# Kernel optimization log

Hardware: AMD Instinct MI355X
Metric: run time of the kernel (lower is better)

The kernel has to match this reference:

```python
import jax, jax.numpy as jnp
import numpy as np

N = 50000
E = 1600000
IN_C = 128
HID = 128
OUT_C = 64


def setup_inputs() -> dict:
    key = jax.random.key(0)
    ks = jax.random.split(key, 10)
    x = jax.random.normal(ks[0], (N, IN_C), dtype=jnp.float32)
    edge_index = jax.random.randint(ks[1], (2, E), 0, N, dtype=jnp.int64)
    s = lambda fan_in: 1.0 / np.sqrt(fan_in)
    W1 = jax.random.uniform(ks[2], (HID, IN_C), jnp.float32, -s(IN_C), s(IN_C))
    b1 = jnp.zeros((HID,), jnp.float32)
    Wc = jax.random.uniform(ks[3], (HID, HID + IN_C), jnp.float32, -s(HID + IN_C), s(HID + IN_C))
    bc = jax.random.uniform(ks[4], (HID,), jnp.float32, -s(HID + IN_C), s(HID + IN_C))
    W2 = jax.random.uniform(ks[5], (HID, HID), jnp.float32, -s(HID), s(HID))
    b2 = jnp.zeros((HID,), jnp.float32)
    Wo = jax.random.uniform(ks[6], (OUT_C, 2 * HID), jnp.float32, -s(2 * HID), s(2 * HID))
    bo = jax.random.uniform(ks[7], (OUT_C,), jnp.float32, -s(2 * HID), s(2 * HID))
    return {"x": x, "edge_index": edge_index, "W1": W1, "b1": b1,
            "Wc": Wc, "bc": bc, "W2": W2, "b2": b2, "Wo": Wo, "bo": bo}


def _gcn_conv(x, src, dst, norm, W, b):
    # PyG GCNConv: h = x @ W^T, propagate with sym-norm coeffs, add bias.
    h = x @ W.T                                   # [N, F_out]
    msg = h[src] * norm[:, None]                  # gather + scale, [E+N, F_out]
    out = jax.ops.segment_sum(msg, dst, num_segments=N)  # scatter-add
    return out + b


def _norm_coeffs(edge_index):
    # add self-loops, then sym normalization: D^{-1/2} A_hat D^{-1/2}
    loop = jnp.arange(N, dtype=edge_index.dtype)
    src = jnp.concatenate([edge_index[0], loop])
    dst = jnp.concatenate([edge_index[1], loop])
    deg = jax.ops.segment_sum(jnp.ones_like(dst, dtype=jnp.float32), dst, num_segments=N)
    dis = jnp.where(deg > 0, jax.lax.rsqrt(deg), 0.0)
    norm = dis[src] * dis[dst]
    return src, dst, norm


def reference(x, edge_index, W1, b1, Wc, bc, W2, b2, Wo, bo):
    src, dst, norm = _norm_coeffs(edge_index)
    x_agg = jax.nn.relu(_gcn_conv(x, src, dst, norm, W1, b1))
    x_comb = jnp.concatenate([x_agg, x], axis=1)
    x_comb = jax.nn.relu(x_comb @ Wc.T + bc)
    # dropout is identity in eval mode
    x_agg2 = _gcn_conv(x_comb, src, dst, norm, W2, b2)
    x_out = jnp.concatenate([x_agg2, x_comb], axis=1)
    return x_out @ Wo.T + bo
```

## Files before the change

### kernel.cpp

```cpp
#include <hip/hip_runtime.h>
#include <hip/hip_fp16.h>

#define Nn 50000
#define Ee 1600000
#define NRANGE 196
#define CAP 10240
#define CHUNK 4096

typedef __attribute__((ext_vector_type(8))) short short8;
typedef __attribute__((ext_vector_type(4))) float f32x4;
typedef unsigned short ushort;
typedef unsigned int uint;

__device__ __forceinline__ ushort f32_to_bf16(float f) {
    unsigned u = __builtin_bit_cast(unsigned, f);
    unsigned r = u + 0x7FFFu + ((u >> 16) & 1u);
    return (ushort)(r >> 16);
}
__device__ __forceinline__ float bf16_to_f32(ushort h) {
    unsigned u = ((unsigned)h) << 16;
    return __builtin_bit_cast(float, u);
}


__global__ __launch_bounds__(256) void partition_kernel(const int* __restrict__ ei,
                                                        int* __restrict__ gcursor,
                                                        int2* __restrict__ buckets) {
    __shared__ int cnt[NRANGE];
    __shared__ int cur[NRANGE];
    int t = threadIdx.x;
    if (t < NRANGE) cnt[t] = 0;
    __syncthreads();
    int base = blockIdx.x * CHUNK;
    const int* __restrict__ dst = ei + Ee;
    #pragma unroll
    for (int k = 0; k < CHUNK / 256; ++k) {
        int e = base + k * 256 + t;
        if (e < Ee) atomicAdd(&cnt[dst[e] >> 8], 1);
    }
    __syncthreads();
    if (t < NRANGE) cur[t] = atomicAdd(&gcursor[t], cnt[t]);
    __syncthreads();
    #pragma unroll
    for (int k = 0; k < CHUNK / 256; ++k) {
        int e = base + k * 256 + t;
        if (e < Ee) {
            int d = dst[e];
            int r = d >> 8;
            int slot = atomicAdd(&cur[r], 1);
            if (slot < CAP) buckets[r * CAP + slot] = make_int2(ei[e], d);
        }
    }
}

__global__ __launch_bounds__(256) void count_kernel(const int2* __restrict__ buckets,
                                                    const int* __restrict__ gcursor,
                                                    int* __restrict__ counts,
                                                    float* __restrict__ dis) {
    __shared__ int cnt[256];
    int r = blockIdx.x, t = threadIdx.x;
    cnt[t] = 0;
    __syncthreads();
    int n = gcursor[r]; n = (n < CAP) ? n : CAP;
    const int2* b = buckets + (size_t)r * CAP;
    for (int i = t; i < n; i += 256) {
        int2 p = b[i];
        atomicAdd(&cnt[p.y & 255], 1);
    }
    __syncthreads();
    int node = r * 256 + t;
    if (node < Nn) {
        counts[node] = cnt[t];
        dis[node] = rsqrtf((float)(cnt[t] + 1));
    }
}

__global__ void scan1_kernel(const int* __restrict__ counts, int* __restrict__ offsets,
                             int* __restrict__ partials) {
    __shared__ int sd[256];
    int t = threadIdx.x;
    int i = blockIdx.x * 256 + t;
    int cp = 0;
    if (i < Nn) cp = (counts[i] + 7) & ~7;
    int v = cp;
    #pragma unroll
    for (int off = 1; off < 256; off <<= 1) {
        sd[t] = v; __syncthreads();
        int add = (t >= off) ? sd[t - off] : 0;
        __syncthreads();
        v += add;
    }
    if (i < Nn) offsets[i] = v - cp;
    if (t == 255) partials[blockIdx.x] = v;
}

__global__ void scan3_kernel(int* __restrict__ offsets, const int* __restrict__ partials,
                             const int* __restrict__ counts, int* __restrict__ csr) {
    __shared__ int sd[256];
    int t = threadIdx.x;
    int s = (t < blockIdx.x) ? partials[t] : 0;
    sd[t] = s; __syncthreads();
    #pragma unroll
    for (int off = 128; off > 0; off >>= 1) {
        if (t < off) sd[t] += sd[t + off];
        __syncthreads();
    }
    int base = sd[0];
    int i = blockIdx.x * 256 + t;
    if (i < Nn) {
        int off = offsets[i] + base;
        offsets[i] = off;
        int deg = counts[i];
        int cp  = (deg + 7) & ~7;
        for (int j = off + deg; j < off + cp; ++j) csr[j] = Nn;
        if (i == Nn - 1) offsets[Nn] = off + cp;
    }
}

__global__ __launch_bounds__(256) void fill_kernel(const int2* __restrict__ buckets,
                                                   const int* __restrict__ gcursor,
                                                   const int* __restrict__ offsets,
                                                   int* __restrict__ csr) {
    __shared__ int cur[256];
    int r = blockIdx.x, t = threadIdx.x;
    int node = r * 256 + t;
    cur[t] = (node < Nn) ? offsets[node] : 0;
    __syncthreads();
    int n = gcursor[r]; n = (n < CAP) ? n : CAP;
    const int2* b = buckets + (size_t)r * CAP;
    for (int i = t; i < n; i += 256) {
        int2 p = b[i];
        int pos = atomicAdd(&cur[p.y & 255], 1);
        csr[pos] = p.x;
    }
}

__global__ void prep_w_kernel(const float* __restrict__ W1, const float* __restrict__ Wc,
                              const float* __restrict__ W2, const float* __restrict__ Wo,
                              ushort* __restrict__ base) {
    int i = blockIdx.x * 256 + threadIdx.x;
    const float* src; ushort* hi; ushort* lo; int idx;
    if (i < 16384)      { src = W1; hi = base;          lo = base + 16384;  idx = i; }
    else if (i < 49152) { src = Wc; hi = base + 32768;  lo = base + 65536;  idx = i - 16384; }
    else if (i < 65536) { src = W2; hi = base + 98304;  lo = base + 114688; idx = i - 49152; }
    else                { src = Wo; hi = base + 131072; lo = base + 147456; idx = i - 65536; }
    float f = src[idx];
    ushort hb = f32_to_bf16(f);
    hi[idx] = hb;
    lo[idx] = f32_to_bf16(f - bf16_to_f32(hb));
}

__global__ void split_x_kernel(const float* __restrict__ x, ushort* __restrict__ xhi,
                               ushort* __restrict__ xlo) {
    int i = (blockIdx.x * 256 + threadIdx.x) * 4;
    float4 v = *(const float4*)(x + i);
    float vv[4] = {v.x, v.y, v.z, v.w};
    ushort h[4], l[4];
    #pragma unroll
    for (int j = 0; j < 4; ++j) {
        h[j] = f32_to_bf16(vv[j]);
        l[j] = f32_to_bf16(vv[j] - bf16_to_f32(h[j]));
    }
    *(uint2*)(xhi + i) = make_uint2((uint)h[0] | ((uint)h[1] << 16),
                                    (uint)h[2] | ((uint)h[3] << 16));
    *(uint2*)(xlo + i) = make_uint2((uint)l[0] | ((uint)l[1] << 16),
                                    (uint)l[2] | ((uint)l[3] << 16));
}

template <int CO, int K, bool RELU, bool HASBIAS, bool SCALEDIS, int OUTMODE>
__global__ __launch_bounds__(256, 3) void mfma_gemm(
    const ushort* __restrict__ AH0, const ushort* __restrict__ AL0,
    const ushort* __restrict__ AH1, const ushort* __restrict__ AL1,
    const ushort* __restrict__ Whi, const ushort* __restrict__ Wlo,
    const float* __restrict__ bias, const float* __restrict__ dis,
    void* __restrict__ outp, ushort* __restrict__ outLo) {
    constexpr int NF = CO / 16;
    constexpr int NCH = K / 64;
    constexpr int WISS = CO / 32;

    __shared__ ushort lds[2 * 64 * 64 + 2 * CO * 64];
    ushort* ldsAh = lds;
    ushort* ldsAl = lds + 64 * 64;
    ushort* ldsWh = lds + 2 * 64 * 64;
    ushort* ldsWl = ldsWh + CO * 64;

    int tid  = threadIdx.x;
    int wave = tid >> 6;
    int lane = tid & 63;
    int c = lane & 15;
    int g = lane >> 4;
    int row0 = blockIdx.x * 64;

    f32x4 acc1[NF], acc2[NF];
    #pragma unroll
    for (int f = 0; f < NF; ++f) {
        acc1[f] = (f32x4){0.f, 0.f, 0.f, 0.f};
        acc2[f] = (f32x4){0.f, 0.f, 0.f, 0.f};
    }

    #pragma unroll
    for (int ch = 0; ch < NCH; ++ch) {
        const int k0 = ch * 64;
        const ushort* Ah = (K == 256 && k0 >= 128) ? AH1 : AH0;
        const ushort* Al = (K == 256 && k0 >= 128) ? AL1 : AL0;
        const int kb = (K == 256 && k0 >= 128) ? (k0 - 128) : k0;

        #pragma unroll
        for (int i = 0; i < 2; ++i) {
            int idx = tid + i * 256;
            int row = idx >> 3, kg = idx & 7;
            int gr = row0 + row; gr = (gr < Nn) ? gr : (Nn - 1);
            int sb = (kg * 16) ^ ((row & 7) << 4);
            int ldsoff = (i * 256 + wave * 64) * 8;
            __builtin_amdgcn_global_load_lds(Ah + (size_t)gr * 128 + kb + (sb >> 1),
                                             &ldsAh[ldsoff], 16, 0, 0);
            __builtin_amdgcn_global_load_lds(Al + (size_t)gr * 128 + kb + (sb >> 1),
                                             &ldsAl[ldsoff], 16, 0, 0);
        }
        #pragma unroll
        for (int i = 0; i < WISS; ++i) {
            int idx = tid + i * 256;
            int col = idx >> 3, kg = idx & 7;
            int sb = (kg * 16) ^ ((col & 7) << 4);
            int ldsoff = (i * 256 + wave * 64) * 8;
            __builtin_amdgcn_global_load_lds(Whi + (size_t)col * K + k0 + (sb >> 1),
                                             &ldsWh[ldsoff], 16, 0, 0);
            __builtin_amdgcn_global_load_lds(Wlo + (size_t)col * K + k0 + (sb >> 1),
                                             &ldsWl[ldsoff], 16, 0, 0);
        }
        __syncthreads();

        #pragma unroll
        for (int s = 0; s < 2; ++s) {
            int arow = wave * 16 + c;
            int ab = (s * 64 + g * 16) ^ ((arow & 7) << 4);
            short8 ahi = *(const short8*)((const char*)ldsAh + arow * 128 + ab);
            short8 alo = *(const short8*)((const char*)ldsAl + arow * 128 + ab);
            #pragma unroll
            for (int f = 0; f < NF; ++f) {
                int col = f * 16 + c;
                int wb = (s * 64 + g * 16) ^ ((col & 7) << 4);
                short8 bh = *(const short8*)((const char*)ldsWh + col * 128 + wb);
                short8 bl = *(const short8*)((const char*)ldsWl + col * 128 + wb);
                acc1[f] = __builtin_amdgcn_mfma_f32_16x16x32_bf16(ahi, bh, acc1[f], 0, 0, 0);
                acc2[f] = __builtin_amdgcn_mfma_f32_16x16x32_bf16(ahi, bl, acc2[f], 0, 0, 0);
                acc2[f] = __builtin_amdgcn_mfma_f32_16x16x32_bf16(alo, bh, acc2[f], 0, 0, 0);
            }
        }
        __syncthreads();
    }

    #pragma unroll
    for (int f = 0; f < NF; ++f) {
        int col = f * 16 + c;
        float bv = HASBIAS ? bias[col] : 0.f;
        #pragma unroll
        for (int rg = 0; rg < 4; ++rg) {
            int row = row0 + wave * 16 + g * 4 + rg;
            if (row < Nn) {
                float v = acc1[f][rg] + acc2[f][rg] + bv;
                if (RELU) v = fmaxf(v, 0.f);
                if (SCALEDIS) v *= dis[row];
                size_t idx = (size_t)row * CO + col;
                if constexpr (OUTMODE == 1) {
                    ((__half*)outp)[idx] = __float2half_rn(v);
                } else if constexpr (OUTMODE == 2) {
                    ushort hb = f32_to_bf16(v);
                    ((ushort*)outp)[idx] = hb;
                    outLo[idx] = f32_to_bf16(v - bf16_to_f32(hb));
                } else {
                    ((float*)outp)[idx] = v;
                }
            }
        }
    }
}

template <bool RELU>
__global__ __launch_bounds__(256) void propagate_kernel(
    const __half* __restrict__ gbuf, const int* __restrict__ offs,
    const int* __restrict__ csr, const float* __restrict__ dis,
    const float* __restrict__ bias, ushort* __restrict__ outHi,
    ushort* __restrict__ outLo) {
    int node = blockIdx.x * 4 + (threadIdx.x >> 6);
    if (node >= Nn) return;
    int lane = threadIdx.x & 63;
    float2 sv = __half22float2(*((const __half2*)(gbuf + ((size_t)node << 7)) + lane));
    float ax = sv.x, ay = sv.y;
    int beg = offs[node], end = offs[node + 1];
    for (int e = beg; e < end; e += 8) {
        int s0 = csr[e],     s1 = csr[e + 1], s2 = csr[e + 2], s3 = csr[e + 3];
        int s4 = csr[e + 4], s5 = csr[e + 5], s6 = csr[e + 6], s7 = csr[e + 7];
        __half2 h0 = *((const __half2*)(gbuf + ((size_t)s0 << 7)) + lane);
        __half2 h1 = *((const __half2*)(gbuf + ((size_t)s1 << 7)) + lane);
        __half2 h2 = *((const __half2*)(gbuf + ((size_t)s2 << 7)) + lane);
        __half2 h3 = *((const __half2*)(gbuf + ((size_t)s3 << 7)) + lane);
        __half2 h4 = *((const __half2*)(gbuf + ((size_t)s4 << 7)) + lane);
        __half2 h5 = *((const __half2*)(gbuf + ((size_t)s5 << 7)) + lane);
        __half2 h6 = *((const __half2*)(gbuf + ((size_t)s6 << 7)) + lane);
        __half2 h7 = *((const __half2*)(gbuf + ((size_t)s7 << 7)) + lane);
        float2 v0 = __half22float2(h0), v1 = __half22float2(h1);
        float2 v2 = __half22float2(h2), v3 = __half22float2(h3);
        float2 v4 = __half22float2(h4), v5 = __half22float2(h5);
        float2 v6 = __half22float2(h6), v7 = __half22float2(h7);
        ax += ((v0.x + v1.x) + (v2.x + v3.x)) + ((v4.x + v5.x) + (v6.x + v7.x));
        ay += ((v0.y + v1.y) + (v2.y + v3.y)) + ((v4.y + v5.y) + (v6.y + v7.y));
    }
    float di = dis[node];
    ax = fmaf(di, ax, bias[lane * 2]);
    ay = fmaf(di, ay, bias[lane * 2 + 1]);
    if (RELU) { ax = fmaxf(ax, 0.f); ay = fmaxf(ay, 0.f); }
    ushort hx = f32_to_bf16(ax), hy = f32_to_bf16(ay);
    ushort lx = f32_to_bf16(ax - bf16_to_f32(hx));
    ushort ly = f32_to_bf16(ay - bf16_to_f32(hy));
    ((uint*)(outHi + ((size_t)node << 7)))[lane] = (uint)hx | ((uint)hy << 16);
    ((uint*)(outLo + ((size_t)node << 7)))[lane] = (uint)lx | ((uint)ly << 16);
}


extern "C" void kernel_launch(void* const* d_in, const int* in_sizes, int n_in,
                              void* d_out, int out_size, void* d_ws, size_t ws_size,
                              hipStream_t stream) {
    const float* x  = (const float*)d_in[0];
    const int*   ei = (const int*)d_in[1];
    const float* W1 = (const float*)d_in[2];
    const float* b1 = (const float*)d_in[3];
    const float* Wc = (const float*)d_in[4];
    const float* bc = (const float*)d_in[5];
    const float* W2 = (const float*)d_in[6];
    const float* b2 = (const float*)d_in[7];
    const float* Wo = (const float*)d_in[8];
    const float* bo = (const float*)d_in[9];
    float* out = (float*)d_out;

    char* base = (char*)d_ws;
    auto carve = [&](size_t bytes) {
        void* p = (void*)base;
        base += (bytes + 255) & ~(size_t)255;
        return p;
    };
    char*  tmp      = (char*)carve(512 * 1024);
    int*   gcursor  = (int*)tmp;
    int*   counts   = (int*)(tmp + 1024);
    ushort* wplanes = (ushort*)tmp;
    int*   offsets  = (int*)carve((Nn + 1) * sizeof(int));
    int*   partials = (int*)carve(256 * sizeof(int));
    float* dis      = (float*)carve(Nn * sizeof(float));
    int2*  buckets  = (int2*)carve((size_t)NRANGE * CAP * sizeof(int2));
    int*   csr      = (int*)carve(((size_t)Ee + 8 * Nn) * sizeof(int));
    __half* gbuf    = (__half*)carve((size_t)(Nn + 2) * 128 * sizeof(__half));
    ushort* xhi     = (ushort*)carve((size_t)Nn * 128 * sizeof(ushort));
    ushort* xlo     = (ushort*)carve((size_t)Nn * 128 * sizeof(ushort));
    ushort* aggHi   = (ushort*)carve((size_t)Nn * 128 * sizeof(ushort));
    ushort* aggLo   = (ushort*)carve((size_t)Nn * 128 * sizeof(ushort));
    ushort* combHi  = (ushort*)carve((size_t)Nn * 128 * sizeof(ushort));
    ushort* combLo  = (ushort*)carve((size_t)Nn * 128 * sizeof(ushort));

    const ushort* w1hi = wplanes;
    const ushort* w1lo = wplanes + 16384;
    const ushort* wchi = wplanes + 32768;
    const ushort* wclo = wplanes + 65536;
    const ushort* w2hi = wplanes + 98304;
    const ushort* w2lo = wplanes + 114688;
    const ushort* wohi = wplanes + 131072;
    const ushort* wolo = wplanes + 147456;

    const int SCAN_BLOCKS = (Nn + 255) / 256;
    const int PBLOCKS = (Ee + CHUNK - 1) / CHUNK;

    hipMemsetAsync(gcursor, 0, NRANGE * sizeof(int), stream);
    hipMemsetAsync(gbuf + (size_t)Nn * 128, 0, 256, stream);
    partition_kernel<<<PBLOCKS, 256, 0, stream>>>(ei, gcursor, buckets);
    count_kernel<<<NRANGE, 256, 0, stream>>>(buckets, gcursor, counts, dis);
    scan1_kernel<<<SCAN_BLOCKS, 256, 0, stream>>>(counts, offsets, partials);
    scan3_kernel<<<SCAN_BLOCKS, 256, 0, stream>>>(offsets, partials, counts, csr);
    fill_kernel<<<NRANGE, 256, 0, stream>>>(buckets, gcursor, offsets, csr);

    prep_w_kernel<<<320, 256, 0, stream>>>(W1, Wc, W2, Wo, (ushort*)wplanes);
    split_x_kernel<<<6250, 256, 0, stream>>>(x, xhi, xlo);

    const int GB = (Nn + 63) / 64;
    const int PB = (Nn + 3) / 4;

    mfma_gemm<128, 128, false, false, true, 1><<<GB, 256, 0, stream>>>(
        xhi, xlo, nullptr, nullptr, w1hi, w1lo, nullptr, dis, gbuf, nullptr);
    propagate_kernel<true><<<PB, 256, 0, stream>>>(gbuf, offsets, csr, dis, b1, aggHi, aggLo);
    mfma_gemm<128, 256, true, true, false, 2><<<GB, 256, 0, stream>>>(
        aggHi, aggLo, xhi, xlo, wchi, wclo, bc, nullptr, combHi, combLo);
    mfma_gemm<128, 128, false, false, true, 1><<<GB, 256, 0, stream>>>(
        combHi, combLo, nullptr, nullptr, w2hi, w2lo, nullptr, dis, gbuf, nullptr);
    propagate_kernel<false><<<PB, 256, 0, stream>>>(gbuf, offsets, csr, dis, b2, aggHi, aggLo);
    mfma_gemm<64, 256, false, true, false, 0><<<GB, 256, 0, stream>>>(
        aggHi, aggLo, combHi, combLo, wohi, wolo, bo, nullptr, out, nullptr);
}
```

Measured before the change: 339.9 us.

## Fuse sparse propagation into following concat GEMM via LDS-resident aggregated tile

Each propagate kernel is merged with the GEMM that consumes its output. A block of four waves aggregates 64 nodes (16 per wave) and writes the bf16 hi/lo result straight into a swizzled LDS tile. The GEMM then reads its first K half from that tile and streams the second half (x or comb) from global memory. This removes the write and re-read of the aggregation buffers and two launches, but propagation parallelism drops from one node per wave across 12500 blocks to 16 serial nodes per wave across 782 blocks, with higher LDS use.

```diff
diff --git a/kernel.cpp b/kernel.cpp
--- a/kernel.cpp
+++ b/kernel.cpp
@@ -170,7 +170,6 @@
 template <int CO, int K, bool RELU, bool HASBIAS, bool SCALEDIS, int OUTMODE>
 __global__ __launch_bounds__(256, 3) void mfma_gemm(
     const ushort* __restrict__ AH0, const ushort* __restrict__ AL0,
-    const ushort* __restrict__ AH1, const ushort* __restrict__ AL1,
     const ushort* __restrict__ Whi, const ushort* __restrict__ Wlo,
     const float* __restrict__ bias, const float* __restrict__ dis,
     void* __restrict__ outp, ushort* __restrict__ outLo) {
@@ -201,10 +200,6 @@
     #pragma unroll
     for (int ch = 0; ch < NCH; ++ch) {
         const int k0 = ch * 64;
-        const ushort* Ah = (K == 256 && k0 >= 128) ? AH1 : AH0;
-        const ushort* Al = (K == 256 && k0 >= 128) ? AL1 : AL0;
-        const int kb = (K == 256 && k0 >= 128) ? (k0 - 128) : k0;
-
         #pragma unroll
         for (int i = 0; i < 2; ++i) {
             int idx = tid + i * 256;
@@ -212,9 +207,9 @@
             int gr = row0 + row; gr = (gr < Nn) ? gr : (Nn - 1);
             int sb = (kg * 16) ^ ((row & 7) << 4);
             int ldsoff = (i * 256 + wave * 64) * 8;
-            __builtin_amdgcn_global_load_lds(Ah + (size_t)gr * 128 + kb + (sb >> 1),
+            __builtin_amdgcn_global_load_lds(AH0 + (size_t)gr * 128 + k0 + (sb >> 1),
                                              &ldsAh[ldsoff], 16, 0, 0);
-            __builtin_amdgcn_global_load_lds(Al + (size_t)gr * 128 + kb + (sb >> 1),
+            __builtin_amdgcn_global_load_lds(AL0 + (size_t)gr * 128 + k0 + (sb >> 1),
                                              &ldsAl[ldsoff], 16, 0, 0);
         }
         #pragma unroll
@@ -276,45 +271,157 @@
     }
 }
 
-template <bool RELU>
-__global__ __launch_bounds__(256) void propagate_kernel(
+template <int CO, bool RELUP, bool RELUG, int OUTMODE>
+__global__ __launch_bounds__(256, 2) void fused_prop_gemm(
     const __half* __restrict__ gbuf, const int* __restrict__ offs,
     const int* __restrict__ csr, const float* __restrict__ dis,
-    const float* __restrict__ bias, ushort* __restrict__ outHi,
-    ushort* __restrict__ outLo) {
-    int node = blockIdx.x * 4 + (threadIdx.x >> 6);
-    if (node >= Nn) return;
-    int lane = threadIdx.x & 63;
-    float2 sv = __half22float2(*((const __half2*)(gbuf + ((size_t)node << 7)) + lane));
-    float ax = sv.x, ay = sv.y;
-    int beg = offs[node], end = offs[node + 1];
-    for (int e = beg; e < end; e += 8) {
-        int s0 = csr[e],     s1 = csr[e + 1], s2 = csr[e + 2], s3 = csr[e + 3];
-        int s4 = csr[e + 4], s5 = csr[e + 5], s6 = csr[e + 6], s7 = csr[e + 7];
-        __half2 h0 = *((const __half2*)(gbuf + ((size_t)s0 << 7)) + lane);
-        __half2 h1 = *((const __half2*)(gbuf + ((size_t)s1 << 7)) + lane);
-        __half2 h2 = *((const __half2*)(gbuf + ((size_t)s2 << 7)) + lane);
-        __half2 h3 = *((const __half2*)(gbuf + ((size_t)s3 << 7)) + lane);
-        __half2 h4 = *((const __half2*)(gbuf + ((size_t)s4 << 7)) + lane);
-        __half2 h5 = *((const __half2*)(gbuf + ((size_t)s5 << 7)) + lane);
-        __half2 h6 = *((const __half2*)(gbuf + ((size_t)s6 << 7)) + lane);
-        __half2 h7 = *((const __half2*)(gbuf + ((size_t)s7 << 7)) + lane);
-        float2 v0 = __half22float2(h0), v1 = __half22float2(h1);
-        float2 v2 = __half22float2(h2), v3 = __half22float2(h3);
-        float2 v4 = __half22float2(h4), v5 = __half22float2(h5);
-        float2 v6 = __half22float2(h6), v7 = __half22float2(h7);
-        ax += ((v0.x + v1.x) + (v2.x + v3.x)) + ((v4.x + v5.x) + (v6.x + v7.x));
-        ay += ((v0.y + v1.y) + (v2.y + v3.y)) + ((v4.y + v5.y) + (v6.y + v7.y));
-    }
-    float di = dis[node];
-    ax = fmaf(di, ax, bias[lane * 2]);
-    ay = fmaf(di, ay, bias[lane * 2 + 1]);
-    if (RELU) { ax = fmaxf(ax, 0.f); ay = fmaxf(ay, 0.f); }
-    ushort hx = f32_to_bf16(ax), hy = f32_to_bf16(ay);
-    ushort lx = f32_to_bf16(ax - bf16_to_f32(hx));
-    ushort ly = f32_to_bf16(ay - bf16_to_f32(hy));
-    ((uint*)(outHi + ((size_t)node << 7)))[lane] = (uint)hx | ((uint)hy << 16);
-    ((uint*)(outLo + ((size_t)node << 7)))[lane] = (uint)lx | ((uint)ly << 16);
+    const float* __restrict__ biasP,
+    const ushort* __restrict__ AH1, const ushort* __restrict__ AL1,
+    const ushort* __restrict__ Whi, const ushort* __restrict__ Wlo,
+    const float* __restrict__ biasG,
+    void* __restrict__ outp, ushort* __restrict__ outLo) {
+    constexpr int NF = CO / 16;
+    constexpr int WISS = CO / 32;
+
+    __shared__ ushort lds[2 * 64 * 128 + 2 * CO * 64];
+    ushort* tileAh = lds;
+    ushort* tileAl = lds + 64 * 128;
+    ushort* stgAh  = lds;
+    ushort* stgAl  = lds + 64 * 64;
+    ushort* stgWh  = lds + 2 * 64 * 128;
+    ushort* stgWl  = stgWh + CO * 64;
+
+    int tid  = threadIdx.x;
+    int wave = tid >> 6;
+    int lane = tid & 63;
+    int c = lane & 15;
+    int g = lane >> 4;
+    int row0 = blockIdx.x * 64;
+
+    for (int i = 0; i < 16; ++i) {
+        int r = wave * 16 + i;
+        int node = row0 + r;
+        int n = (node < Nn) ? node : (Nn - 1);
+        float2 sv = __half22float2(*((const __half2*)(gbuf + ((size_t)n << 7)) + lane));
+        float ax = sv.x, ay = sv.y;
+        int beg = offs[n], end = offs[n + 1];
+        for (int e = beg; e < end; e += 8) {
+            int s0 = csr[e],     s1 = csr[e + 1], s2 = csr[e + 2], s3 = csr[e + 3];
+            int s4 = csr[e + 4], s5 = csr[e + 5], s6 = csr[e + 6], s7 = csr[e + 7];
+            __half2 h0 = *((const __half2*)(gbuf + ((size_t)s0 << 7)) + lane);
+            __half2 h1 = *((const __half2*)(gbuf + ((size_t)s1 << 7)) + lane);
+            __half2 h2 = *((const __half2*)(gbuf + ((size_t)s2 << 7)) + lane);
+            __half2 h3 = *((const __half2*)(gbuf + ((size_t)s3 << 7)) + lane);
+            __half2 h4 = *((const __half2*)(gbuf + ((size_t)s4 << 7)) + lane);
+            __half2 h5 = *((const __half2*)(gbuf + ((size_t)s5 << 7)) + lane);
+            __half2 h6 = *((const __half2*)(gbuf + ((size_t)s6 << 7)) + lane);
+            __half2 h7 = *((const __half2*)(gbuf + ((size_t)s7 << 7)) + lane);
+            float2 v0 = __half22float2(h0), v1 = __half22float2(h1);
+            float2 v2 = __half22float2(h2), v3 = __half22float2(h3);
+            float2 v4 = __half22float2(h4), v5 = __half22float2(h5);
+            float2 v6 = __half22float2(h6), v7 = __half22float2(h7);
+            ax += ((v0.x + v1.x) + (v2.x + v3.x)) + ((v4.x + v5.x) + (v6.x + v7.x));
+            ay += ((v0.y + v1.y) + (v2.y + v3.y)) + ((v4.y + v5.y) + (v6.y + v7.y));
+        }
+        float di = dis[n];
+        ax = fmaf(di, ax, biasP[lane * 2]);
+        ay = fmaf(di, ay, biasP[lane * 2 + 1]);
+        if (RELUP) { ax = fmaxf(ax, 0.f); ay = fmaxf(ay, 0.f); }
+        ushort hx = f32_to_bf16(ax), hy = f32_to_bf16(ay);
+        ushort lx = f32_to_bf16(ax - bf16_to_f32(hx));
+        ushort ly = f32_to_bf16(ay - bf16_to_f32(hy));
+        int sb = (4 * lane) ^ ((r & 7) << 4);
+        *(uint*)((char*)tileAh + r * 256 + sb) = (uint)hx | ((uint)hy << 16);
+        *(uint*)((char*)tileAl + r * 256 + sb) = (uint)lx | ((uint)ly << 16);
+    }
+    __syncthreads();
+
+    f32x4 acc1[NF], acc2[NF];
+    #pragma unroll
+    for (int f = 0; f < NF; ++f) {
+        acc1[f] = (f32x4){0.f, 0.f, 0.f, 0.f};
+        acc2[f] = (f32x4){0.f, 0.f, 0.f, 0.f};
+    }
+
+    #pragma unroll
+    for (int ch = 0; ch < 4; ++ch) {
+        const int k0 = ch * 64;
+        if (ch >= 2) {
+            const int kb = k0 - 128;
+            #pragma unroll
+            for (int i = 0; i < 2; ++i) {
+                int idx = tid + i * 256;
+                int row = idx >> 3, kg = idx & 7;
+                int gr = row0 + row; gr = (gr < Nn) ? gr : (Nn - 1);
+                int sb = (kg * 16) ^ ((row & 7) << 4);
+                int ldsoff = (i * 256 + wave * 64) * 8;
+                __builtin_amdgcn_global_load_lds(AH1 + (size_t)gr * 128 + kb + (sb >> 1),
+                                                 &stgAh[ldsoff], 16, 0, 0);
+                __builtin_amdgcn_global_load_lds(AL1 + (size_t)gr * 128 + kb + (sb >> 1),
+                                                 &stgAl[ldsoff], 16, 0, 0);
+            }
+        }
+        #pragma unroll
+        for (int i = 0; i < WISS; ++i) {
+            int idx = tid + i * 256;
+            int col = idx >> 3, kg = idx & 7;
+            int sb = (kg * 16) ^ ((col & 7) << 4);
+            int ldsoff = (i * 256 + wave * 64) * 8;
+            __builtin_amdgcn_global_load_lds(Whi + (size_t)col * 256 + k0 + (sb >> 1),
+                                             &stgWh[ldsoff], 16, 0, 0);
+            __builtin_amdgcn_global_load_lds(Wlo + (size_t)col * 256 + k0 + (sb >> 1),
+                                             &stgWl[ldsoff], 16, 0, 0);
+        }
+        __syncthreads();
+
+        #pragma unroll
+        for (int s = 0; s < 2; ++s) {
+            int arow = wave * 16 + c;
+            short8 ahi, alo;
+            if (ch < 2) {
+                int ab = (ch * 128 + s * 64 + g * 16) ^ ((arow & 7) << 4);
+                ahi = *(const short8*)((const char*)tileAh + arow * 256 + ab);
+                alo = *(const short8*)((const char*)tileAl + arow * 256 + ab);
+            } else {
+                int ab = (s * 64 + g * 16) ^ ((arow & 7) << 4);
+                ahi = *(const short8*)((const char*)stgAh + arow * 128 + ab);
+                alo = *(const short8*)((const char*)stgAl + arow * 128 + ab);
+            }
+            #pragma unroll
+            for (int f = 0; f < NF; ++f) {
+                int col = f * 16 + c;
+                int wb = (s * 64 + g * 16) ^ ((col & 7) << 4);
+                short8 bh = *(const short8*)((const char*)stgWh + col * 128 + wb);
+                short8 bl = *(const short8*)((const char*)stgWl + col * 128 + wb);
+                acc1[f] = __builtin_amdgcn_mfma_f32_16x16x32_bf16(ahi, bh, acc1[f], 0, 0, 0);
+                acc2[f] = __builtin_amdgcn_mfma_f32_16x16x32_bf16(ahi, bl, acc2[f], 0, 0, 0);
+                acc2[f] = __builtin_amdgcn_mfma_f32_16x16x32_bf16(alo, bh, acc2[f], 0, 0, 0);
+            }
+        }
+        __syncthreads();
+    }
+
+    #pragma unroll
+    for (int f = 0; f < NF; ++f) {
+        int col = f * 16 + c;
+        float bv = biasG[col];
+        #pragma unroll
+        for (int rg = 0; rg < 4; ++rg) {
+            int row = row0 + wave * 16 + g * 4 + rg;
+            if (row < Nn) {
+                float v = acc1[f][rg] + acc2[f][rg] + bv;
+                if (RELUG) v = fmaxf(v, 0.f);
+                size_t idx = (size_t)row * CO + col;
+                if constexpr (OUTMODE == 2) {
+                    ushort hb = f32_to_bf16(v);
+                    ((ushort*)outp)[idx] = hb;
+                    outLo[idx] = f32_to_bf16(v - bf16_to_f32(hb));
+                } else {
+                    ((float*)outp)[idx] = v;
+                }
+            }
+        }
+    }
 }
 
 
@@ -351,8 +458,6 @@
     __half* gbuf    = (__half*)carve((size_t)(Nn + 2) * 128 * sizeof(__half));
     ushort* xhi     = (ushort*)carve((size_t)Nn * 128 * sizeof(ushort));
     ushort* xlo     = (ushort*)carve((size_t)Nn * 128 * sizeof(ushort));
-    ushort* aggHi   = (ushort*)carve((size_t)Nn * 128 * sizeof(ushort));
-    ushort* aggLo   = (ushort*)carve((size_t)Nn * 128 * sizeof(ushort));
     ushort* combHi  = (ushort*)carve((size_t)Nn * 128 * sizeof(ushort));
     ushort* combLo  = (ushort*)carve((size_t)Nn * 128 * sizeof(ushort));
 
@@ -380,16 +485,13 @@
     split_x_kernel<<<6250, 256, 0, stream>>>(x, xhi, xlo);
 
     const int GB = (Nn + 63) / 64;
-    const int PB = (Nn + 3) / 4;
 
     mfma_gemm<128, 128, false, false, true, 1><<<GB, 256, 0, stream>>>(
-        xhi, xlo, nullptr, nullptr, w1hi, w1lo, nullptr, dis, gbuf, nullptr);
-    propagate_kernel<true><<<PB, 256, 0, stream>>>(gbuf, offsets, csr, dis, b1, aggHi, aggLo);
-    mfma_gemm<128, 256, true, true, false, 2><<<GB, 256, 0, stream>>>(
-        aggHi, aggLo, xhi, xlo, wchi, wclo, bc, nullptr, combHi, combLo);
+        xhi, xlo, w1hi, w1lo, nullptr, dis, gbuf, nullptr);
+    fused_prop_gemm<128, true, true, 2><<<GB, 256, 0, stream>>>(
+        gbuf, offsets, csr, dis, b1, xhi, xlo, wchi, wclo, bc, combHi, combLo);
     mfma_gemm<128, 128, false, false, true, 1><<<GB, 256, 0, stream>>>(
-        combHi, combLo, nullptr, nullptr, w2hi, w2lo, nullptr, dis, gbuf, nullptr);
-    propagate_kernel<false><<<PB, 256, 0, stream>>>(gbuf, offsets, csr, dis, b2, aggHi, aggLo);
-    mfma_gemm<64, 256, false, true, false, 0><<<GB, 256, 0, stream>>>(
-        aggHi, aggLo, combHi, combLo, wohi, wolo, bo, nullptr, out, nullptr);
-}
+        combHi, combLo, w2hi, w2lo, nullptr, dis, gbuf, nullptr);
+    fused_prop_gemm<64, false, false, 0><<<GB, 256, 0, stream>>>(
+        gbuf, offsets, csr, dis, b2, combHi, combLo, wohi, wolo, bo, out, nullptr);
+}
```

Measured after the change: 476.3 us. 1.4x slower.
